# Performance work log

Hardware: AMD Instinct MI355X
Metric: run time of the kernel (lower is better)

Reference implementation:

```python
import jax, jax.numpy as jnp
import numpy as np

B, IN, HID, OUT, G = 16384, 1024, 2048, 256, 8


def _linear_init(key, fan_in, shape):
    bound = 1.0 / np.sqrt(fan_in)
    return jax.random.uniform(key, shape, jnp.float32, -bound, bound)


def setup_inputs() -> dict:
    key = jax.random.key(0)
    ks = jax.random.split(key, 10)
    x = jax.random.normal(ks[0], (B, IN), jnp.float32)
    gid = jax.random.randint(ks[1], (B,), 0, G)
    # stacked per-group head params (out_heads + final_out)
    W1 = _linear_init(ks[2], IN, (G, IN, HID))
    b1 = _linear_init(ks[3], IN, (G, HID))
    W2 = _linear_init(ks[4], HID, (G, HID, OUT))
    b2 = _linear_init(ks[5], HID, (G, OUT))
    # generic_out params
    Wg1 = _linear_init(ks[6], IN, (IN, HID))
    bg1 = _linear_init(ks[7], IN, (HID,))
    Wg2 = _linear_init(ks[8], HID, (HID, OUT))
    bg2 = _linear_init(ks[9], HID, (OUT,))
    return {"x": x, "gid": gid, "W1": W1, "b1": b1, "W2": W2, "b2": b2,
            "Wg1": Wg1, "bg1": bg1, "Wg2": Wg2, "bg2": bg2}


def reference(x, gid, W1, b1, W2, b2, Wg1, bg1, Wg2, bg2):
    # generic path (applied to every sample, as in the torch loop)
    gen_out = jax.nn.relu(x @ Wg1 + bg1) @ Wg2 + bg2  # [B, OUT]
    # routed path: loop over the small fixed number of groups (grouped-GEMM style),
    # selecting each sample's result by its group id.
    out = jnp.zeros_like(gen_out)
    for g in range(W1.shape[0]):
        h = jax.nn.relu(x @ W1[g] + b1[g])         # [B, HID]
        o = h @ W2[g] + b2[g]                       # [B, OUT]
        out = jnp.where((gid == g)[:, None], o, out)
    return out, gen_out
```

## Files before the change

### kernel.cpp

```cpp
#include <hip/hip_runtime.h>
#include <cstdint>
#include <cstddef>

static constexpr int Bn   = 16384;
static constexpr int INn  = 1024;
static constexpr int HIDn = 2048;
static constexpr int OUTn = 256;
static constexpr int NGn  = 8;
static constexpr int MAXT = 136;
static constexpr int NBLK = Bn / 256;

typedef __attribute__((ext_vector_type(8))) __bf16 bf16x8;
typedef __attribute__((ext_vector_type(4))) float  f32x4;

__device__ __forceinline__ unsigned short f2bf(float f) {
  unsigned int u = __builtin_bit_cast(unsigned int, f);
  u += 0x7fffu + ((u >> 16) & 1u);
  return (unsigned short)(u >> 16);
}

__device__ __forceinline__ void load_lds16(const void* g, void* l) {
  __builtin_amdgcn_global_load_lds(
      (const __attribute__((address_space(1))) unsigned int*)g,
      (__attribute__((address_space(3))) unsigned int*)l, 16, 0, 0);
}

__global__ void blkhist_k(const int* __restrict__ gid, int* __restrict__ blk_cnt) {
  __shared__ int h[NGn];
  if (threadIdx.x < NGn) h[threadIdx.x] = 0;
  __syncthreads();
  atomicAdd(&h[gid[blockIdx.x * 256 + threadIdx.x]], 1);
  __syncthreads();
  if (threadIdx.x < NGn) blk_cnt[blockIdx.x * NGn + threadIdx.x] = h[threadIdx.x];
}

__global__ void scan_desc_k(const int* __restrict__ blk_cnt, int* __restrict__ cnt,
                            int* __restrict__ goff, int* __restrict__ ntl,
                            int2* __restrict__ desc, int* __restrict__ bbase) {
  __shared__ int s[NGn][NBLK];
  __shared__ int tot[NGn], go[NGn];
  int t = threadIdx.x;
  int g = t >> 6, b = t & 63;
  s[g][b] = blk_cnt[b * NGn + g];
  __syncthreads();
  int pre = 0;
  for (int b2 = 0; b2 < b; b2++) pre += s[g][b2];
  if (b == 63) tot[g] = pre + s[g][63];
  __syncthreads();
  if (t == 0) {
    int o = 0, nt = 0;
    for (int gg = 0; gg < NGn; gg++) {
      go[gg] = o; goff[gg] = o; cnt[gg] = tot[gg];
      for (int m = 0; m < tot[gg]; m += 128) { desc[nt].x = gg; desc[nt].y = m; nt++; }
      o += tot[gg];
    }
    *ntl = nt;
  }
  __syncthreads();
  bbase[b * NGn + g] = go[g] + pre;
}

__global__ void place_k(const int* __restrict__ gid, const int* __restrict__ bbase,
                        int* __restrict__ ridx) {
  __shared__ int wcnt[4][NGn];
  int i = blockIdx.x * 256 + threadIdx.x;
  int g = gid[i];
  int lane = threadIdx.x & 63, w = threadIdx.x >> 6;
  unsigned long long mym = 0;
  #pragma unroll
  for (int grp = 0; grp < NGn; grp++) {
    unsigned long long m = __ballot(g == grp);
    if (lane == 0) wcnt[w][grp] = __popcll(m);
    if (g == grp) mym = m;
  }
  __syncthreads();
  int wrank = __popcll(mym & ((1ull << lane) - 1ull));
  int base = 0;
  for (int w2 = 0; w2 < w; w2++) base += wcnt[w2][g];
  ridx[bbase[blockIdx.x * NGn + g] + base + wrank] = i;
}

__global__ void conv_bf16_k(const float* __restrict__ src, unsigned short* __restrict__ dst,
                            int nvec) {
  int i = blockIdx.x * blockDim.x + threadIdx.x;
  int stride = gridDim.x * blockDim.x;
  for (; i < nvec; i += stride) {
    float4 v = ((const float4*)src)[i];
    uint2 o;
    o.x = (unsigned)f2bf(v.x) | ((unsigned)f2bf(v.y) << 16);
    o.y = (unsigned)f2bf(v.z) | ((unsigned)f2bf(v.w) << 16);
    ((uint2*)dst)[i] = o;
  }
}

__global__ void transpose_k(const float* __restrict__ src, unsigned short* __restrict__ dst,
                            int K, int N) {
  __shared__ float t[32][33];
  size_t bo = (size_t)blockIdx.z * (size_t)K * (size_t)N;
  int n0 = blockIdx.x * 32, k0 = blockIdx.y * 32;
  #pragma unroll
  for (int i = 0; i < 32; i += 8)
    t[threadIdx.y + i][threadIdx.x] =
        src[bo + (size_t)(k0 + threadIdx.y + i) * N + n0 + threadIdx.x];
  __syncthreads();
  #pragma unroll
  for (int i = 0; i < 32; i += 8)
    dst[bo + (size_t)(n0 + threadIdx.y + i) * K + k0 + threadIdx.x] =
        f2bf(t[threadIdx.x][threadIdx.y + i]);
}

#define STAGE(U, KT, BUFP) do {                                        \
    load_lds16(gp[(U)*2+0] + (KT)*64, (BUFP) + loff[(U)*2+0]);         \
    load_lds16(gp[(U)*2+1] + (KT)*64, (BUFP) + loff[(U)*2+1]); } while (0)

__global__ __launch_bounds__(512, 2) void g8gen_k(
    const unsigned short* __restrict__ A, const unsigned short* __restrict__ Bt,
    const float* __restrict__ bias, unsigned short* __restrict__ Cout) {
  constexpr int K = INn;
  constexpr int N = HIDn;
  constexpr int NT = K / 64;

  int mtile, ntile;
  {
    int gx = gridDim.x;
    int nwg = gx * gridDim.y;
    int l = blockIdx.y * gx + blockIdx.x;
    int q = nwg >> 3;
    int xcd = l & 7, i = l >> 3;
    int sl = xcd * q + i;
    mtile = sl / gx; ntile = sl - mtile * gx;
  }
  const int row0 = mtile * 256, n0 = ntile * 256;

  __shared__ __align__(16) char lds[131072];

  const int t = threadIdx.x, lane = t & 63, wid = t >> 6;
  const int wm = wid >> 2, wn = wid & 3;
  const int ln15 = lane & 15, l16 = lane >> 4, ln7 = lane & 7;

  const unsigned short* gp[8];
  int loff[8];
  #pragma unroll
  for (int u = 0; u < 4; u++) {
    #pragma unroll
    for (int j = 0; j < 2; j++) {
      int c = j * 512 + t;
      int rl = c >> 3, gg = c & 7;
      int r;
      if (u == 0)      r = rl + ((rl & 64) ? 64 : 0);
      else if (u == 1) r = 64 + rl + ((rl & 64) ? 64 : 0);
      else {
        r = ((rl >> 5) << 6) + (rl & 31);
        if (u == 3) r += 32;
      }
      int gsrcg = gg ^ (r & 7);
      if (u < 2) gp[u * 2 + j] = A + (size_t)(row0 + r) * K + gsrcg * 8;
      else       gp[u * 2 + j] = Bt + (size_t)(n0 + r) * K + gsrcg * 8;
      int rl0 = j * 64 + wid * 8;
      int r0;
      if (u == 0)      r0 = rl0 + ((rl0 & 64) ? 64 : 0);
      else if (u == 1) r0 = 64 + rl0 + ((rl0 & 64) ? 64 : 0);
      else {
        r0 = ((rl0 >> 5) << 6) + (rl0 & 31);
        if (u == 3) r0 += 32;
      }
      loff[u * 2 + j] = (u < 2 ? 0 : 32768) + r0 * 128;
    }
  }

  int arow[8], brow[4];
  #pragma unroll
  for (int m = 0; m < 8; m++) arow[m] = (wm * 128 + m * 16 + ln15) << 7;
  #pragma unroll
  for (int n = 0; n < 4; n++) brow[n] = 32768 + ((wn * 64 + n * 16 + ln15) << 7);
  const int g0 = (l16 ^ ln7) << 4;
  const int g1 = ((4 + l16) ^ ln7) << 4;

  f32x4 acc[8][4];
  #pragma unroll
  for (int m = 0; m < 8; m++)
    #pragma unroll
    for (int n = 0; n < 4; n++) acc[m][n] = {0.f, 0.f, 0.f, 0.f};

  char* const buf0 = lds;
  char* const buf1 = lds + 65536;

  STAGE(0, 0, buf0); STAGE(2, 0, buf0); STAGE(3, 0, buf0); STAGE(1, 0, buf0);
  STAGE(0, 1, buf1); STAGE(2, 1, buf1); STAGE(3, 1, buf1);
  asm volatile("s_waitcnt vmcnt(6)" ::: "memory");
  __builtin_amdgcn_s_barrier();

  bf16x8 avL[4][2], avH[4][2], bvL[2][2], bvH[2][2];

  auto KTILE = [&](int tt, char* bufc, char* bufn) {
    const int kc1 = tt + 1 < NT ? tt + 1 : NT - 1;
    const int kc2 = tt + 2 < NT ? tt + 2 : NT - 1;
    #pragma unroll
    for (int m = 0; m < 4; m++) {
      avL[m][0] = *(const bf16x8*)(bufc + arow[m] + g0);
      avL[m][1] = *(const bf16x8*)(bufc + arow[m] + g1);
    }
    #pragma unroll
    for (int n = 0; n < 2; n++) {
      bvL[n][0] = *(const bf16x8*)(bufc + brow[n] + g0);
      bvL[n][1] = *(const bf16x8*)(bufc + brow[n] + g1);
    }
    STAGE(1, kc1, bufn);
    __builtin_amdgcn_s_barrier();
    asm volatile("s_waitcnt lgkmcnt(0)" ::: "memory");
    __builtin_amdgcn_s_setprio(1);
    #pragma unroll
    for (int ks = 0; ks < 2; ks++)
      #pragma unroll
      for (int m = 0; m < 4; m++)
        #pragma unroll
        for (int n = 0; n < 2; n++)
          acc[m][n] = __builtin_amdgcn_mfma_f32_16x16x32_bf16(avL[m][ks], bvL[n][ks], acc[m][n], 0, 0, 0);
    __builtin_amdgcn_s_setprio(0);
    __builtin_amdgcn_s_barrier();
    #pragma unroll
    for (int n = 0; n < 2; n++) {
      bvH[n][0] = *(const bf16x8*)(bufc + brow[2 + n] + g0);
      bvH[n][1] = *(const bf16x8*)(bufc + brow[2 + n] + g1);
    }
    STAGE(0, kc2, bufc);
    __builtin_amdgcn_s_barrier();
    asm volatile("s_waitcnt lgkmcnt(0)" ::: "memory");
    __builtin_amdgcn_s_setprio(1);
    #pragma unroll
    for (int ks = 0; ks < 2; ks++)
      #pragma unroll
      for (int m = 0; m < 4; m++)
        #pragma unroll
        for (int n = 0; n < 2; n++)
          acc[m][2 + n] = __builtin_amdgcn_mfma_f32_16x16x32_bf16(avL[m][ks], bvH[n][ks], acc[m][2 + n], 0, 0, 0);
    __builtin_amdgcn_s_setprio(0);
    __builtin_amdgcn_s_barrier();
    #pragma unroll
    for (int m = 0; m < 4; m++) {
      avH[m][0] = *(const bf16x8*)(bufc + arow[4 + m] + g0);
      avH[m][1] = *(const bf16x8*)(bufc + arow[4 + m] + g1);
    }
    STAGE(2, kc2, bufc);
    __builtin_amdgcn_s_barrier();
    asm volatile("s_waitcnt lgkmcnt(0)" ::: "memory");
    __builtin_amdgcn_s_setprio(1);
    #pragma unroll
    for (int ks = 0; ks < 2; ks++)
      #pragma unroll
      for (int m = 0; m < 4; m++)
        #pragma unroll
        for (int n = 0; n < 2; n++)
          acc[4 + m][2 + n] = __builtin_amdgcn_mfma_f32_16x16x32_bf16(avH[m][ks], bvH[n][ks], acc[4 + m][2 + n], 0, 0, 0);
    __builtin_amdgcn_s_setprio(0);
    __builtin_amdgcn_s_barrier();
    STAGE(3, kc2, bufc);
    asm volatile("s_waitcnt vmcnt(6)" ::: "memory");
    __builtin_amdgcn_s_barrier();
    __builtin_amdgcn_s_setprio(1);
    #pragma unroll
    for (int ks = 0; ks < 2; ks++)
      #pragma unroll
      for (int m = 0; m < 4; m++)
        #pragma unroll
        for (int n = 0; n < 2; n++)
          acc[4 + m][n] = __builtin_amdgcn_mfma_f32_16x16x32_bf16(avH[m][ks], bvL[n][ks], acc[4 + m][n], 0, 0, 0);
    __builtin_amdgcn_s_setprio(0);
    __builtin_amdgcn_s_barrier();
  };

  for (int it = 0; it < NT; it += 2) {
    KTILE(it, buf0, buf1);
    KTILE(it + 1, buf1, buf0);
  }

  float biasv[4];
  #pragma unroll
  for (int n = 0; n < 4; n++) biasv[n] = bias[n0 + wn * 64 + n * 16 + ln15];
  #pragma unroll
  for (int m = 0; m < 8; m++) {
    #pragma unroll
    for (int j = 0; j < 4; j++) {
      size_t orow = (size_t)(row0 + wm * 128 + m * 16 + l16 * 4 + j);
      #pragma unroll
      for (int n = 0; n < 4; n++) {
        float v = acc[m][n][j] + biasv[n];
        v = v > 0.f ? v : 0.f;
        Cout[orow * N + n0 + wn * 64 + n * 16 + ln15] = f2bf(v);
      }
    }
  }
}
#undef STAGE

template <bool GROUPED, bool GATHER_A, int OMODE>
__device__ __forceinline__ void gemm_body(
    const unsigned short* __restrict__ A, const unsigned short* __restrict__ Bt,
    const float* __restrict__ bias, void* __restrict__ Cout, int K, int N,
    int ksplit, size_t zstride,
    const int* __restrict__ cnt, const int* __restrict__ goff,
    const int* __restrict__ ntiles, const int2* __restrict__ desc,
    const int* __restrict__ ridx) {
  int mtile, ntile;
  {
    int gx = gridDim.x;
    int nwg = gx * gridDim.y;
    int l = blockIdx.y * gx + blockIdx.x;
    int q = nwg >> 3, rm = nwg & 7;
    int xcd = l & 7, i = l >> 3;
    int sl = (xcd < rm ? xcd * (q + 1) : rm * (q + 1) + (xcd - rm) * q) + i;
    mtile = sl / gx; ntile = sl - mtile * gx;
  }

  int row0, cnt_rem;
  if constexpr (GROUPED) {
    if (mtile >= *ntiles) return;
    int2 d = desc[mtile];
    int g = d.x;
    row0 = goff[g] + d.y;
    cnt_rem = cnt[g] - d.y;
    Bt += (size_t)g * (size_t)K * (size_t)N;
    if constexpr (OMODE == 0) bias += (size_t)g * (size_t)N;
  } else {
    row0 = mtile * 128;
    cnt_rem = 128;
  }
  int n0 = ntile * 128;
  const int kbase = blockIdx.z * ksplit;

  __shared__ __align__(16) char lds[32768];

  int t = threadIdx.x;
  int lane = t & 63, wid = t >> 6;

  const unsigned short* pA[4];
  const unsigned short* pB[4];
  #pragma unroll
  for (int i = 0; i < 4; i++) {
    int r = i * 32 + (t >> 3);
    int cg = (t & 7) ^ (r & 7);
    int rA;
    if constexpr (GROUPED) {
      int rcl = r < cnt_rem ? r : cnt_rem - 1;
      if constexpr (GATHER_A) rA = ridx[row0 + rcl];
      else                    rA = row0 + rcl;
    } else {
      rA = row0 + r;
    }
    pA[i] = A + (size_t)rA * K + cg * 8;
    pB[i] = Bt + (size_t)(n0 + r) * K + cg * 8;
  }

  int ln15 = lane & 15, l16 = lane >> 4, ln7 = lane & 7;
  int wm = wid >> 1, wn = wid & 1;
  int aoffb[4], boffb[4];
  #pragma unroll
  for (int m = 0; m < 4; m++) aoffb[m] = (wm * 64 + m * 16 + ln15) << 7;
  #pragma unroll
  for (int n = 0; n < 4; n++) boffb[n] = ((wn * 64 + n * 16 + ln15) << 7) + 16384;
  const int gsw0 = (l16 ^ ln7) << 4;
  const int gsw1 = ((4 + l16) ^ ln7) << 4;

  f32x4 acc[4][4];
  #pragma unroll
  for (int m = 0; m < 4; m++)
    #pragma unroll
    for (int n = 0; n < 4; n++) acc[m][n] = {0.f, 0.f, 0.f, 0.f};

  for (int kt = kbase; kt < kbase + ksplit; kt += 64) {
    __syncthreads();
    #pragma unroll
    for (int i = 0; i < 4; i++)
      load_lds16(pA[i] + kt, lds + i * 4096 + wid * 1024);
    #pragma unroll
    for (int i = 0; i < 4; i++)
      load_lds16(pB[i] + kt, lds + 16384 + i * 4096 + wid * 1024);
    __syncthreads();
    #pragma unroll
    for (int ks = 0; ks < 2; ks++) {
      const int gsw = ks ? gsw1 : gsw0;
      bf16x8 av[4], bv[4];
      #pragma unroll
      for (int m = 0; m < 4; m++) av[m] = *(const bf16x8*)(lds + aoffb[m] + gsw);
      #pragma unroll
      for (int n = 0; n < 4; n++) bv[n] = *(const bf16x8*)(lds + boffb[n] + gsw);
      #pragma unroll
      for (int m = 0; m < 4; m++)
        #pragma unroll
        for (int n = 0; n < 4; n++)
          acc[m][n] = __builtin_amdgcn_mfma_f32_16x16x32_bf16(av[m], bv[n], acc[m][n], 0, 0, 0);
    }
  }

  float biasv[4];
  if constexpr (OMODE == 0) {
    #pragma unroll
    for (int n = 0; n < 4; n++) biasv[n] = bias[n0 + wn * 64 + n * 16 + ln15];
  }
  float* Po = (float*)Cout + (size_t)blockIdx.z * zstride;

  #pragma unroll
  for (int m = 0; m < 4; m++) {
    #pragma unroll
    for (int j = 0; j < 4; j++) {
      int r = wm * 64 + m * 16 + l16 * 4 + j;
      if (GROUPED && r >= cnt_rem) continue;
      size_t orow = (size_t)(row0 + r);
      #pragma unroll
      for (int n = 0; n < 4; n++) {
        int col = n0 + wn * 64 + n * 16 + ln15;
        if constexpr (OMODE == 0) {
          float v = acc[m][n][j] + biasv[n];
          v = v > 0.f ? v : 0.f;
          ((unsigned short*)Cout)[orow * N + col] = f2bf(v);
        } else {
          Po[orow * N + col] = acc[m][n][j];
        }
      }
    }
  }
}

__global__ __launch_bounds__(256, 2) void g1rt_k(
    const unsigned short* A, const unsigned short* Bt, const float* bias, void* C,
    int K, int N, int ksplit, size_t zs,
    const int* cnt, const int* goff, const int* ntl, const int2* desc, const int* ridx) {
  gemm_body<true, true, 0>(A, Bt, bias, C, K, N, ksplit, zs, cnt, goff, ntl, desc, ridx);
}
__global__ __launch_bounds__(256, 2) void g2gen_k(
    const unsigned short* A, const unsigned short* Bt, const float* bias, void* C,
    int K, int N, int ksplit, size_t zs,
    const int* cnt, const int* goff, const int* ntl, const int2* desc, const int* ridx) {
  gemm_body<false, false, 1>(A, Bt, bias, C, K, N, ksplit, zs, cnt, goff, ntl, desc, ridx);
}
__global__ __launch_bounds__(256, 2) void g2rt_k(
    const unsigned short* A, const unsigned short* Bt, const float* bias, void* C,
    int K, int N, int ksplit, size_t zs,
    const int* cnt, const int* goff, const int* ntl, const int2* desc, const int* ridx) {
  gemm_body<true, false, 1>(A, Bt, bias, C, K, N, ksplit, zs, cnt, goff, ntl, desc, ridx);
}

__global__ void redu_gen_k(const float* __restrict__ P, const float* __restrict__ bias,
                           float* __restrict__ outp) {
  int i = blockIdx.x * 256 + threadIdx.x;
  float4 a = ((const float4*)P)[i];
  float4 b = ((const float4*)(P + (size_t)Bn * OUTn))[i];
  int c4 = (i & 63) << 2;
  float4 bv = *(const float4*)(bias + c4);
  ((float4*)outp)[i] = {a.x + b.x + bv.x, a.y + b.y + bv.y,
                        a.z + b.z + bv.z, a.w + b.w + bv.w};
}

__global__ void redu_rt_k(const float* __restrict__ P, const float* __restrict__ b2,
                          float* __restrict__ outp,
                          const int* __restrict__ cnt, const int* __restrict__ goff,
                          const int* __restrict__ ntl, const int2* __restrict__ desc,
                          const int* __restrict__ ridx) {
  if ((int)blockIdx.x >= *ntl) return;
  int2 d = desc[blockIdx.x];
  int g = d.x;
  int row0 = goff[g] + d.y;
  int rem = cnt[g] - d.y; if (rem > 128) rem = 128;
  int t = threadIdx.x;
  int c4 = (t & 63) << 2;
  float4 bv = *(const float4*)(b2 + (size_t)g * OUTn + c4);
  for (int r = t >> 6; r < rem; r += 4) {
    size_t src = (size_t)(row0 + r) * OUTn + c4;
    float4 a = *(const float4*)(P + src);
    float4 b = *(const float4*)(P + (size_t)Bn * OUTn + src);
    int orow = ridx[row0 + r];
    *(float4*)(outp + (size_t)orow * OUTn + c4) =
        {a.x + b.x + bv.x, a.y + b.y + bv.y, a.z + b.z + bv.z, a.w + b.w + bv.w};
  }
}

extern "C" void kernel_launch(void* const* d_in, const int* in_sizes, int n_in,
                              void* d_out, int out_size, void* d_ws, size_t ws_size,
                              hipStream_t stream) {
  const float* x   = (const float*)d_in[0];
  const int*   gid = (const int*)d_in[1];
  const float* W1  = (const float*)d_in[2];
  const float* b1  = (const float*)d_in[3];
  const float* W2  = (const float*)d_in[4];
  const float* b2  = (const float*)d_in[5];
  const float* Wg1 = (const float*)d_in[6];
  const float* bg1 = (const float*)d_in[7];
  const float* Wg2 = (const float*)d_in[8];
  const float* bg2 = (const float*)d_in[9];

  float* out = (float*)d_out;
  float* gen = out + (size_t)Bn * OUTn;

  char* ws = (char*)d_ws;
  unsigned short* xb   = (unsigned short*)(ws);
  unsigned short* W1t  = (unsigned short*)(ws + 33554432);
  float*          Ppar = (float*)(ws + 33554432);
  unsigned short* W2t  = (unsigned short*)(ws + 67108864);
  unsigned short* Wg1t = (unsigned short*)(ws + 75497472);
  unsigned short* Wg2t = (unsigned short*)(ws + 79691776);
  unsigned short* h    = (unsigned short*)(ws + 80740352);
  int* ridx            = (int*)(ws + 147849216);
  int* meta            = (int*)(ws + 147914752);
  int* cnt   = meta;
  int* goff  = meta + 8;
  int* ntl   = meta + 16;
  int2* desc = (int2*)(meta + 32);
  int* blk_cnt = meta + 512;
  int* bbase   = meta + 1024;

  const size_t zstr = (size_t)Bn * OUTn;

  blkhist_k<<<NBLK, 256, 0, stream>>>(gid, blk_cnt);
  scan_desc_k<<<1, 512, 0, stream>>>(blk_cnt, cnt, goff, ntl, desc, bbase);
  place_k<<<NBLK, 256, 0, stream>>>(gid, bbase, ridx);

  conv_bf16_k<<<2048, 256, 0, stream>>>(x, xb, Bn * INn / 4);
  dim3 tb(32, 8);
  transpose_k<<<dim3(HIDn / 32, INn / 32, NGn), tb, 0, stream>>>(W1, W1t, INn, HIDn);
  transpose_k<<<dim3(OUTn / 32, HIDn / 32, NGn), tb, 0, stream>>>(W2, W2t, HIDn, OUTn);
  transpose_k<<<dim3(HIDn / 32, INn / 32, 1), tb, 0, stream>>>(Wg1, Wg1t, INn, HIDn);
  transpose_k<<<dim3(OUTn / 32, HIDn / 32, 1), tb, 0, stream>>>(Wg2, Wg2t, HIDn, OUTn);

  g1rt_k<<<dim3(HIDn / 128, MAXT), 256, 0, stream>>>(
      xb, W1t, b1, h, INn, HIDn, INn, 0, cnt, goff, ntl, desc, ridx);
  g2rt_k<<<dim3(OUTn / 128, MAXT, 2), 256, 0, stream>>>(
      h, W2t, nullptr, Ppar, HIDn, OUTn, HIDn / 2, zstr, cnt, goff, ntl, desc, ridx);
  redu_rt_k<<<MAXT, 256, 0, stream>>>(Ppar, b2, out, cnt, goff, ntl, desc, ridx);

  g8gen_k<<<dim3(HIDn / 256, Bn / 256), 512, 0, stream>>>(xb, Wg1t, bg1, h);
  g2gen_k<<<dim3(OUTn / 128, Bn / 128, 2), 256, 0, stream>>>(
      h, Wg2t, nullptr, Ppar, HIDn, OUTn, HIDn / 2, zstr, nullptr, nullptr, nullptr, nullptr, nullptr);
  redu_gen_k<<<(Bn * OUTn / 4) / 256, 256, 0, stream>>>(Ppar, bg2, gen);
}
```

Measured before the change: 294.7 us.

## Merge transposes and reductions into single launches, prefetch B fragments, raise occupancy

The four weight-transpose launches become one kernel that dispatches on block index, and the two split-K reduction kernels become one kernel. The routed partial buffer stays separate from a new generic partial buffer that reuses the xb workspace region, so both reductions can run together at the end. In g8gen_k the low-half B fragments for the next k-tile are double-buffered and loaded early, before that tile's compute. The grouped GEMM kernels' launch bounds go from 2 to 4 blocks per CU, which may limit registers.

```diff
diff --git a/kernel.cpp b/kernel.cpp
--- a/kernel.cpp
+++ b/kernel.cpp
@@ -93,20 +93,188 @@
   }
 }
 
-__global__ void transpose_k(const float* __restrict__ src, unsigned short* __restrict__ dst,
-                            int K, int N) {
-  __shared__ float t[32][33];
-  size_t bo = (size_t)blockIdx.z * (size_t)K * (size_t)N;
-  int n0 = blockIdx.x * 32, k0 = blockIdx.y * 32;
+__global__ void transposes_k(const float* __restrict__ W1, unsigned short* __restrict__ W1t,
+                             const float* __restrict__ W2, unsigned short* __restrict__ W2t,
+                             const float* __restrict__ Wg1, unsigned short* __restrict__ Wg1t,
+                             const float* __restrict__ Wg2, unsigned short* __restrict__ Wg2t) {
+  __shared__ float tlds[32][33];
+  int bx = blockIdx.x;
+  const float* src; unsigned short* dst;
+  int K, N, nx, ky; size_t bo;
+  if (bx < 16384) {
+    int z = bx >> 11, rem = bx & 2047;
+    nx = rem & 63; ky = rem >> 6; K = INn; N = HIDn;
+    src = W1; dst = W1t; bo = (size_t)z * K * N;
+  } else if (bx < 20480) {
+    int i2 = bx - 16384; int z = i2 >> 9, rem = i2 & 511;
+    nx = rem & 7; ky = rem >> 3; K = HIDn; N = OUTn;
+    src = W2; dst = W2t; bo = (size_t)z * K * N;
+  } else if (bx < 22528) {
+    int i3 = bx - 20480;
+    nx = i3 & 63; ky = i3 >> 6; K = INn; N = HIDn;
+    src = Wg1; dst = Wg1t; bo = 0;
+  } else {
+    int i4 = bx - 22528;
+    nx = i4 & 7; ky = i4 >> 3; K = HIDn; N = OUTn;
+    src = Wg2; dst = Wg2t; bo = 0;
+  }
+  int n0 = nx * 32, k0 = ky * 32;
   #pragma unroll
   for (int i = 0; i < 32; i += 8)
-    t[threadIdx.y + i][threadIdx.x] =
+    tlds[threadIdx.y + i][threadIdx.x] =
         src[bo + (size_t)(k0 + threadIdx.y + i) * N + n0 + threadIdx.x];
   __syncthreads();
   #pragma unroll
   for (int i = 0; i < 32; i += 8)
     dst[bo + (size_t)(n0 + threadIdx.y + i) * K + k0 + threadIdx.x] =
-        f2bf(t[threadIdx.x][threadIdx.y + i]);
+        f2bf(tlds[threadIdx.x][threadIdx.y + i]);
+}
+
+template <bool GROUPED, bool GATHER_A, int OMODE>
+__device__ __forceinline__ void gemm_body(
+    const unsigned short* __restrict__ A, const unsigned short* __restrict__ Bt,
+    const float* __restrict__ bias, void* __restrict__ Cout, int K, int N,
+    int ksplit, size_t zstride,
+    const int* __restrict__ cnt, const int* __restrict__ goff,
+    const int* __restrict__ ntiles, const int2* __restrict__ desc,
+    const int* __restrict__ ridx) {
+  int mtile, ntile;
+  {
+    int gx = gridDim.x;
+    int nwg = gx * gridDim.y;
+    int l = blockIdx.y * gx + blockIdx.x;
+    int q = nwg >> 3, rm = nwg & 7;
+    int xcd = l & 7, i = l >> 3;
+    int sl = (xcd < rm ? xcd * (q + 1) : rm * (q + 1) + (xcd - rm) * q) + i;
+    mtile = sl / gx; ntile = sl - mtile * gx;
+  }
+
+  int row0, cnt_rem;
+  if constexpr (GROUPED) {
+    if (mtile >= *ntiles) return;
+    int2 d = desc[mtile];
+    int g = d.x;
+    row0 = goff[g] + d.y;
+    cnt_rem = cnt[g] - d.y;
+    Bt += (size_t)g * (size_t)K * (size_t)N;
+    if constexpr (OMODE == 0) bias += (size_t)g * (size_t)N;
+  } else {
+    row0 = mtile * 128;
+    cnt_rem = 128;
+  }
+  int n0 = ntile * 128;
+  const int kbase = blockIdx.z * ksplit;
+
+  __shared__ __align__(16) char lds[32768];
+
+  int t = threadIdx.x;
+  int lane = t & 63, wid = t >> 6;
+
+  const unsigned short* pA[4];
+  const unsigned short* pB[4];
+  #pragma unroll
+  for (int i = 0; i < 4; i++) {
+    int r = i * 32 + (t >> 3);
+    int cg = (t & 7) ^ (r & 7);
+    int rA;
+    if constexpr (GROUPED) {
+      int rcl = r < cnt_rem ? r : cnt_rem - 1;
+      if constexpr (GATHER_A) rA = ridx[row0 + rcl];
+      else                    rA = row0 + rcl;
+    } else {
+      rA = row0 + r;
+    }
+    pA[i] = A + (size_t)rA * K + cg * 8;
+    pB[i] = Bt + (size_t)(n0 + r) * K + cg * 8;
+  }
+
+  int ln15 = lane & 15, l16 = lane >> 4, ln7 = lane & 7;
+  int wm = wid >> 1, wn = wid & 1;
+  int aoffb[4], boffb[4];
+  #pragma unroll
+  for (int m = 0; m < 4; m++) aoffb[m] = (wm * 64 + m * 16 + ln15) << 7;
+  #pragma unroll
+  for (int n = 0; n < 4; n++) boffb[n] = ((wn * 64 + n * 16 + ln15) << 7) + 16384;
+  const int gsw0 = (l16 ^ ln7) << 4;
+  const int gsw1 = ((4 + l16) ^ ln7) << 4;
+
+  f32x4 acc[4][4];
+  #pragma unroll
+  for (int m = 0; m < 4; m++)
+    #pragma unroll
+    for (int n = 0; n < 4; n++) acc[m][n] = {0.f, 0.f, 0.f, 0.f};
+
+  for (int kt = kbase; kt < kbase + ksplit; kt += 64) {
+    __syncthreads();
+    #pragma unroll
+    for (int i = 0; i < 4; i++)
+      load_lds16(pA[i] + kt, lds + i * 4096 + wid * 1024);
+    #pragma unroll
+    for (int i = 0; i < 4; i++)
+      load_lds16(pB[i] + kt, lds + 16384 + i * 4096 + wid * 1024);
+    __syncthreads();
+    #pragma unroll
+    for (int ks = 0; ks < 2; ks++) {
+      const int gsw = ks ? gsw1 : gsw0;
+      bf16x8 av[4], bv[4];
+      #pragma unroll
+      for (int m = 0; m < 4; m++) av[m] = *(const bf16x8*)(lds + aoffb[m] + gsw);
+      #pragma unroll
+      for (int n = 0; n < 4; n++) bv[n] = *(const bf16x8*)(lds + boffb[n] + gsw);
+      #pragma unroll
+      for (int m = 0; m < 4; m++)
+        #pragma unroll
+        for (int n = 0; n < 4; n++)
+          acc[m][n] = __builtin_amdgcn_mfma_f32_16x16x32_bf16(av[m], bv[n], acc[m][n], 0, 0, 0);
+    }
+  }
+
+  float biasv[4];
+  if constexpr (OMODE == 0) {
+    #pragma unroll
+    for (int n = 0; n < 4; n++) biasv[n] = bias[n0 + wn * 64 + n * 16 + ln15];
+  }
+  float* Po = (float*)Cout + (size_t)blockIdx.z * zstride;
+
+  #pragma unroll
+  for (int m = 0; m < 4; m++) {
+    #pragma unroll
+    for (int j = 0; j < 4; j++) {
+      int r = wm * 64 + m * 16 + l16 * 4 + j;
+      if (GROUPED && r >= cnt_rem) continue;
+      size_t orow = (size_t)(row0 + r);
+      #pragma unroll
+      for (int n = 0; n < 4; n++) {
+        int col = n0 + wn * 64 + n * 16 + ln15;
+        if constexpr (OMODE == 0) {
+          float v = acc[m][n][j] + biasv[n];
+          v = v > 0.f ? v : 0.f;
+          ((unsigned short*)Cout)[orow * N + col] = f2bf(v);
+        } else {
+          Po[orow * N + col] = acc[m][n][j];
+        }
+      }
+    }
+  }
+}
+
+__global__ __launch_bounds__(256, 4) void g1rt_k(
+    const unsigned short* A, const unsigned short* Bt, const float* bias, void* C,
+    int K, int N, int ksplit, size_t zs,
+    const int* cnt, const int* goff, const int* ntl, const int2* desc, const int* ridx) {
+  gemm_body<true, true, 0>(A, Bt, bias, C, K, N, ksplit, zs, cnt, goff, ntl, desc, ridx);
+}
+__global__ __launch_bounds__(256, 4) void g2gen_k(
+    const unsigned short* A, const unsigned short* Bt, const float* bias, void* C,
+    int K, int N, int ksplit, size_t zs,
+    const int* cnt, const int* goff, const int* ntl, const int2* desc, const int* ridx) {
+  gemm_body<false, false, 1>(A, Bt, bias, C, K, N, ksplit, zs, cnt, goff, ntl, desc, ridx);
+}
+__global__ __launch_bounds__(256, 4) void g2rt_k(
+    const unsigned short* A, const unsigned short* Bt, const float* bias, void* C,
+    int K, int N, int ksplit, size_t zs,
+    const int* cnt, const int* goff, const int* ntl, const int2* desc, const int* ridx) {
+  gemm_body<true, false, 1>(A, Bt, bias, C, K, N, ksplit, zs, cnt, goff, ntl, desc, ridx);
 }
 
 #define STAGE(U, KT, BUFP) do {                                        \
@@ -190,9 +358,16 @@
   asm volatile("s_waitcnt vmcnt(6)" ::: "memory");
   __builtin_amdgcn_s_barrier();
 
-  bf16x8 avL[4][2], avH[4][2], bvL[2][2], bvH[2][2];
-
-  auto KTILE = [&](int tt, char* bufc, char* bufn) {
+  bf16x8 avL[4][2], avH[4][2], bvH[2][2];
+  bf16x8 bvX[2][2], bvY[2][2];
+  #pragma unroll
+  for (int n = 0; n < 2; n++) {
+    bvX[n][0] = *(const bf16x8*)(buf0 + brow[n] + g0);
+    bvX[n][1] = *(const bf16x8*)(buf0 + brow[n] + g1);
+  }
+
+  auto KTILE = [&](int tt, char* bufc, char* bufn,
+                   bf16x8 (&bvC)[2][2], bf16x8 (&bvN)[2][2]) {
     const int kc1 = tt + 1 < NT ? tt + 1 : NT - 1;
     const int kc2 = tt + 2 < NT ? tt + 2 : NT - 1;
     #pragma unroll
@@ -200,11 +375,6 @@
       avL[m][0] = *(const bf16x8*)(bufc + arow[m] + g0);
       avL[m][1] = *(const bf16x8*)(bufc + arow[m] + g1);
     }
-    #pragma unroll
-    for (int n = 0; n < 2; n++) {
-      bvL[n][0] = *(const bf16x8*)(bufc + brow[n] + g0);
-      bvL[n][1] = *(const bf16x8*)(bufc + brow[n] + g1);
-    }
     STAGE(1, kc1, bufn);
     __builtin_amdgcn_s_barrier();
     asm volatile("s_waitcnt lgkmcnt(0)" ::: "memory");
@@ -215,7 +385,7 @@
       for (int m = 0; m < 4; m++)
         #pragma unroll
         for (int n = 0; n < 2; n++)
-          acc[m][n] = __builtin_amdgcn_mfma_f32_16x16x32_bf16(avL[m][ks], bvL[n][ks], acc[m][n], 0, 0, 0);
+          acc[m][n] = __builtin_amdgcn_mfma_f32_16x16x32_bf16(avL[m][ks], bvC[n][ks], acc[m][n], 0, 0, 0);
     __builtin_amdgcn_s_setprio(0);
     __builtin_amdgcn_s_barrier();
     #pragma unroll
@@ -257,6 +427,11 @@
     STAGE(3, kc2, bufc);
     asm volatile("s_waitcnt vmcnt(6)" ::: "memory");
     __builtin_amdgcn_s_barrier();
+    #pragma unroll
+    for (int n = 0; n < 2; n++) {
+      bvN[n][0] = *(const bf16x8*)(bufn + brow[n] + g0);
+      bvN[n][1] = *(const bf16x8*)(bufn + brow[n] + g1);
+    }
     __builtin_amdgcn_s_setprio(1);
     #pragma unroll
     for (int ks = 0; ks < 2; ks++)
@@ -264,14 +439,14 @@
       for (int m = 0; m < 4; m++)
         #pragma unroll
         for (int n = 0; n < 2; n++)
-          acc[4 + m][n] = __builtin_amdgcn_mfma_f32_16x16x32_bf16(avH[m][ks], bvL[n][ks], acc[4 + m][n], 0, 0, 0);
+          acc[4 + m][n] = __builtin_amdgcn_mfma_f32_16x16x32_bf16(avH[m][ks], bvC[n][ks], acc[4 + m][n], 0, 0, 0);
     __builtin_amdgcn_s_setprio(0);
     __builtin_amdgcn_s_barrier();
   };
 
   for (int it = 0; it < NT; it += 2) {
-    KTILE(it, buf0, buf1);
-    KTILE(it + 1, buf1, buf0);
+    KTILE(it, buf0, buf1, bvX, bvY);
+    KTILE(it + 1, buf1, buf0, bvY, bvX);
   }
 
   float biasv[4];
@@ -293,184 +468,39 @@
 }
 #undef STAGE
 
-template <bool GROUPED, bool GATHER_A, int OMODE>
-__device__ __forceinline__ void gemm_body(
-    const unsigned short* __restrict__ A, const unsigned short* __restrict__ Bt,
-    const float* __restrict__ bias, void* __restrict__ Cout, int K, int N,
-    int ksplit, size_t zstride,
-    const int* __restrict__ cnt, const int* __restrict__ goff,
-    const int* __restrict__ ntiles, const int2* __restrict__ desc,
-    const int* __restrict__ ridx) {
-  int mtile, ntile;
-  {
-    int gx = gridDim.x;
-    int nwg = gx * gridDim.y;
-    int l = blockIdx.y * gx + blockIdx.x;
-    int q = nwg >> 3, rm = nwg & 7;
-    int xcd = l & 7, i = l >> 3;
-    int sl = (xcd < rm ? xcd * (q + 1) : rm * (q + 1) + (xcd - rm) * q) + i;
-    mtile = sl / gx; ntile = sl - mtile * gx;
-  }
-
-  int row0, cnt_rem;
-  if constexpr (GROUPED) {
-    if (mtile >= *ntiles) return;
-    int2 d = desc[mtile];
+__global__ void redu_k(const float* __restrict__ Pg, const float* __restrict__ Pr,
+                       const float* __restrict__ bg2, const float* __restrict__ b2,
+                       float* __restrict__ gen, float* __restrict__ outp,
+                       const int* __restrict__ cnt, const int* __restrict__ goff,
+                       const int* __restrict__ ntl, const int2* __restrict__ desc,
+                       const int* __restrict__ ridx) {
+  int bx = blockIdx.x;
+  int t = threadIdx.x;
+  if (bx < 4096) {
+    int i = bx * 256 + t;
+    float4 a = ((const float4*)Pg)[i];
+    float4 b = ((const float4*)(Pg + (size_t)Bn * OUTn))[i];
+    int c4 = (i & 63) << 2;
+    float4 bv = *(const float4*)(bg2 + c4);
+    ((float4*)gen)[i] = {a.x + b.x + bv.x, a.y + b.y + bv.y,
+                         a.z + b.z + bv.z, a.w + b.w + bv.w};
+  } else {
+    int bt = bx - 4096;
+    if (bt >= *ntl) return;
+    int2 d = desc[bt];
     int g = d.x;
-    row0 = goff[g] + d.y;
-    cnt_rem = cnt[g] - d.y;
-    Bt += (size_t)g * (size_t)K * (size_t)N;
-    if constexpr (OMODE == 0) bias += (size_t)g * (size_t)N;
-  } else {
-    row0 = mtile * 128;
-    cnt_rem = 128;
-  }
-  int n0 = ntile * 128;
-  const int kbase = blockIdx.z * ksplit;
-
-  __shared__ __align__(16) char lds[32768];
-
-  int t = threadIdx.x;
-  int lane = t & 63, wid = t >> 6;
-
-  const unsigned short* pA[4];
-  const unsigned short* pB[4];
-  #pragma unroll
-  for (int i = 0; i < 4; i++) {
-    int r = i * 32 + (t >> 3);
-    int cg = (t & 7) ^ (r & 7);
-    int rA;
-    if constexpr (GROUPED) {
-      int rcl = r < cnt_rem ? r : cnt_rem - 1;
-      if constexpr (GATHER_A) rA = ridx[row0 + rcl];
-      else                    rA = row0 + rcl;
-    } else {
-      rA = row0 + r;
-    }
-    pA[i] = A + (size_t)rA * K + cg * 8;
-    pB[i] = Bt + (size_t)(n0 + r) * K + cg * 8;
-  }
-
-  int ln15 = lane & 15, l16 = lane >> 4, ln7 = lane & 7;
-  int wm = wid >> 1, wn = wid & 1;
-  int aoffb[4], boffb[4];
-  #pragma unroll
-  for (int m = 0; m < 4; m++) aoffb[m] = (wm * 64 + m * 16 + ln15) << 7;
-  #pragma unroll
-  for (int n = 0; n < 4; n++) boffb[n] = ((wn * 64 + n * 16 + ln15) << 7) + 16384;
-  const int gsw0 = (l16 ^ ln7) << 4;
-  const int gsw1 = ((4 + l16) ^ ln7) << 4;
-
-  f32x4 acc[4][4];
-  #pragma unroll
-  for (int m = 0; m < 4; m++)
-    #pragma unroll
-    for (int n = 0; n < 4; n++) acc[m][n] = {0.f, 0.f, 0.f, 0.f};
-
-  for (int kt = kbase; kt < kbase + ksplit; kt += 64) {
-    __syncthreads();
-    #pragma unroll
-    for (int i = 0; i < 4; i++)
-      load_lds16(pA[i] + kt, lds + i * 4096 + wid * 1024);
-    #pragma unroll
-    for (int i = 0; i < 4; i++)
-      load_lds16(pB[i] + kt, lds + 16384 + i * 4096 + wid * 1024);
-    __syncthreads();
-    #pragma unroll
-    for (int ks = 0; ks < 2; ks++) {
-      const int gsw = ks ? gsw1 : gsw0;
-      bf16x8 av[4], bv[4];
-      #pragma unroll
-      for (int m = 0; m < 4; m++) av[m] = *(const bf16x8*)(lds + aoffb[m] + gsw);
-      #pragma unroll
-      for (int n = 0; n < 4; n++) bv[n] = *(const bf16x8*)(lds + boffb[n] + gsw);
-      #pragma unroll
-      for (int m = 0; m < 4; m++)
-        #pragma unroll
-        for (int n = 0; n < 4; n++)
-          acc[m][n] = __builtin_amdgcn_mfma_f32_16x16x32_bf16(av[m], bv[n], acc[m][n], 0, 0, 0);
-    }
-  }
-
-  float biasv[4];
-  if constexpr (OMODE == 0) {
-    #pragma unroll
-    for (int n = 0; n < 4; n++) biasv[n] = bias[n0 + wn * 64 + n * 16 + ln15];
-  }
-  float* Po = (float*)Cout + (size_t)blockIdx.z * zstride;
-
-  #pragma unroll
-  for (int m = 0; m < 4; m++) {
-    #pragma unroll
-    for (int j = 0; j < 4; j++) {
-      int r = wm * 64 + m * 16 + l16 * 4 + j;
-      if (GROUPED && r >= cnt_rem) continue;
-      size_t orow = (size_t)(row0 + r);
-      #pragma unroll
-      for (int n = 0; n < 4; n++) {
-        int col = n0 + wn * 64 + n * 16 + ln15;
-        if constexpr (OMODE == 0) {
-          float v = acc[m][n][j] + biasv[n];
-          v = v > 0.f ? v : 0.f;
-          ((unsigned short*)Cout)[orow * N + col] = f2bf(v);
-        } else {
-          Po[orow * N + col] = acc[m][n][j];
-        }
-      }
-    }
-  }
-}
-
-__global__ __launch_bounds__(256, 2) void g1rt_k(
-    const unsigned short* A, const unsigned short* Bt, const float* bias, void* C,
-    int K, int N, int ksplit, size_t zs,
-    const int* cnt, const int* goff, const int* ntl, const int2* desc, const int* ridx) {
-  gemm_body<true, true, 0>(A, Bt, bias, C, K, N, ksplit, zs, cnt, goff, ntl, desc, ridx);
-}
-__global__ __launch_bounds__(256, 2) void g2gen_k(
-    const unsigned short* A, const unsigned short* Bt, const float* bias, void* C,
-    int K, int N, int ksplit, size_t zs,
-    const int* cnt, const int* goff, const int* ntl, const int2* desc, const int* ridx) {
-  gemm_body<false, false, 1>(A, Bt, bias, C, K, N, ksplit, zs, cnt, goff, ntl, desc, ridx);
-}
-__global__ __launch_bounds__(256, 2) void g2rt_k(
-    const unsigned short* A, const unsigned short* Bt, const float* bias, void* C,
-    int K, int N, int ksplit, size_t zs,
-    const int* cnt, const int* goff, const int* ntl, const int2* desc, const int* ridx) {
-  gemm_body<true, false, 1>(A, Bt, bias, C, K, N, ksplit, zs, cnt, goff, ntl, desc, ridx);
-}
-
-__global__ void redu_gen_k(const float* __restrict__ P, const float* __restrict__ bias,
-                           float* __restrict__ outp) {
-  int i = blockIdx.x * 256 + threadIdx.x;
-  float4 a = ((const float4*)P)[i];
-  float4 b = ((const float4*)(P + (size_t)Bn * OUTn))[i];
-  int c4 = (i & 63) << 2;
-  float4 bv = *(const float4*)(bias + c4);
-  ((float4*)outp)[i] = {a.x + b.x + bv.x, a.y + b.y + bv.y,
-                        a.z + b.z + bv.z, a.w + b.w + bv.w};
-}
-
-__global__ void redu_rt_k(const float* __restrict__ P, const float* __restrict__ b2,
-                          float* __restrict__ outp,
-                          const int* __restrict__ cnt, const int* __restrict__ goff,
-                          const int* __restrict__ ntl, const int2* __restrict__ desc,
-                          const int* __restrict__ ridx) {
-  if ((int)blockIdx.x >= *ntl) return;
-  int2 d = desc[blockIdx.x];
-  int g = d.x;
-  int row0 = goff[g] + d.y;
-  int rem = cnt[g] - d.y; if (rem > 128) rem = 128;
-  int t = threadIdx.x;
-  int c4 = (t & 63) << 2;
-  float4 bv = *(const float4*)(b2 + (size_t)g * OUTn + c4);
-  for (int r = t >> 6; r < rem; r += 4) {
-    size_t src = (size_t)(row0 + r) * OUTn + c4;
-    float4 a = *(const float4*)(P + src);
-    float4 b = *(const float4*)(P + (size_t)Bn * OUTn + src);
-    int orow = ridx[row0 + r];
-    *(float4*)(outp + (size_t)orow * OUTn + c4) =
-        {a.x + b.x + bv.x, a.y + b.y + bv.y, a.z + b.z + bv.z, a.w + b.w + bv.w};
+    int row0 = goff[g] + d.y;
+    int rem = cnt[g] - d.y; if (rem > 128) rem = 128;
+    int c4 = (t & 63) << 2;
+    float4 bv = *(const float4*)(b2 + (size_t)g * OUTn + c4);
+    for (int r = t >> 6; r < rem; r += 4) {
+      size_t src = (size_t)(row0 + r) * OUTn + c4;
+      float4 a = *(const float4*)(Pr + src);
+      float4 b = *(const float4*)(Pr + (size_t)Bn * OUTn + src);
+      int orow = ridx[row0 + r];
+      *(float4*)(outp + (size_t)orow * OUTn + c4) =
+          {a.x + b.x + bv.x, a.y + b.y + bv.y, a.z + b.z + bv.z, a.w + b.w + bv.w};
+    }
   }
 }
 
@@ -493,8 +523,9 @@
 
   char* ws = (char*)d_ws;
   unsigned short* xb   = (unsigned short*)(ws);
+  float*          Pgen = (float*)(ws);
   unsigned short* W1t  = (unsigned short*)(ws + 33554432);
-  float*          Ppar = (float*)(ws + 33554432);
+  float*          Prt  = (float*)(ws + 33554432);
   unsigned short* W2t  = (unsigned short*)(ws + 67108864);
   unsigned short* Wg1t = (unsigned short*)(ws + 75497472);
   unsigned short* Wg2t = (unsigned short*)(ws + 79691776);
@@ -515,20 +546,17 @@
   place_k<<<NBLK, 256, 0, stream>>>(gid, bbase, ridx);
 
   conv_bf16_k<<<2048, 256, 0, stream>>>(x, xb, Bn * INn / 4);
-  dim3 tb(32, 8);
-  transpose_k<<<dim3(HIDn / 32, INn / 32, NGn), tb, 0, stream>>>(W1, W1t, INn, HIDn);
-  transpose_k<<<dim3(OUTn / 32, HIDn / 32, NGn), tb, 0, stream>>>(W2, W2t, HIDn, OUTn);
-  transpose_k<<<dim3(HIDn / 32, INn / 32, 1), tb, 0, stream>>>(Wg1, Wg1t, INn, HIDn);
-  transpose_k<<<dim3(OUTn / 32, HIDn / 32, 1), tb, 0, stream>>>(Wg2, Wg2t, HIDn, OUTn);
+  transposes_k<<<23040, dim3(32, 8), 0, stream>>>(W1, W1t, W2, W2t, Wg1, Wg1t, Wg2, Wg2t);
 
   g1rt_k<<<dim3(HIDn / 128, MAXT), 256, 0, stream>>>(
       xb, W1t, b1, h, INn, HIDn, INn, 0, cnt, goff, ntl, desc, ridx);
   g2rt_k<<<dim3(OUTn / 128, MAXT, 2), 256, 0, stream>>>(
-      h, W2t, nullptr, Ppar, HIDn, OUTn, HIDn / 2, zstr, cnt, goff, ntl, desc, ridx);
-  redu_rt_k<<<MAXT, 256, 0, stream>>>(Ppar, b2, out, cnt, goff, ntl, desc, ridx);
+      h, W2t, nullptr, Prt, HIDn, OUTn, HIDn / 2, zstr, cnt, goff, ntl, desc, ridx);
 
   g8gen_k<<<dim3(HIDn / 256, Bn / 256), 512, 0, stream>>>(xb, Wg1t, bg1, h);
   g2gen_k<<<dim3(OUTn / 128, Bn / 128, 2), 256, 0, stream>>>(
-      h, Wg2t, nullptr, Ppar, HIDn, OUTn, HIDn / 2, zstr, nullptr, nullptr, nullptr, nullptr, nullptr);
-  redu_gen_k<<<(Bn * OUTn / 4) / 256, 256, 0, stream>>>(Ppar, bg2, gen);
-}
+      h, Wg2t, nullptr, Pgen, HIDn, OUTn, HIDn / 2, zstr, nullptr, nullptr, nullptr, nullptr, nullptr);
+
+  redu_k<<<4096 + MAXT, 256, 0, stream>>>(Pgen, Prt, bg2, b2, gen, out,
+                                          cnt, goff, ntl, desc, ridx);
+}
```

Measured after the change: 310.5 us. 1.05x slower.
